# Kernel optimization log

Hardware: AMD Instinct MI355X
Metric: run time of the kernel (lower is better)

## Reference

```python
import jax, jax.numpy as jnp
import numpy as np

EMB_DIM = 256
N_EGO = 8192
N_SIDE = 8192
TOP_K = 16


def setup_inputs() -> dict:
    key = jax.random.key(0)
    ks = jax.random.split(key, 9)
    s = 1.0 / np.sqrt(EMB_DIM)
    return {
        "ego_emb": jax.random.normal(ks[0], (N_EGO, EMB_DIM), jnp.float32),
        "side_emb": jax.random.normal(ks[1], (N_SIDE, EMB_DIM), jnp.float32),
        "rel_emb": jax.random.normal(ks[2], (N_SIDE, EMB_DIM), jnp.float32),
        "Wq": jax.random.uniform(ks[3], (EMB_DIM, EMB_DIM), jnp.float32, -s, s),
        "bq": jax.random.uniform(ks[4], (EMB_DIM,), jnp.float32, -s, s),
        "Wk": jax.random.uniform(ks[5], (EMB_DIM, EMB_DIM), jnp.float32, -s, s),
        "bk": jax.random.uniform(ks[6], (EMB_DIM,), jnp.float32, -s, s),
        "Wv": jax.random.uniform(ks[7], (EMB_DIM, EMB_DIM), jnp.float32, -s, s),
        "bv": jax.random.uniform(ks[8], (EMB_DIM,), jnp.float32, -s, s),
    }


def reference(ego_emb, side_emb, rel_emb, Wq, bq, Wk, bk, Wv, bv):
    # Linear projections (torch nn.Linear: x @ W.T + b)
    q = ego_emb @ Wq.T + bq                      # [N_ego, d]
    k = (side_emb * rel_emb) @ Wk.T + bk         # [N_side, d]
    v = side_emb @ Wv.T + bv                     # [N_side, d]

    scale = jnp.sqrt(jnp.asarray(EMB_DIM, q.dtype))
    attn_scores = (q @ k.T) / scale              # [N_ego, N_side] dense

    k_value = min(TOP_K, attn_scores.shape[-1])
    topk_scores, topk_indices = jax.lax.top_k(attn_scores, k_value)  # [N_ego, K]
    attn_weights = jax.nn.softmax(topk_scores, axis=-1)              # [N_ego, K]

    topk_v = v[topk_indices]                     # gather -> [N_ego, K, d]
    aggregated = jnp.sum(topk_v * attn_weights[..., None], axis=1)   # [N_ego, d]
    return aggregated
```

## Files before the change

kernel.cpp:

```cpp
#include <hip/hip_runtime.h>
#include <hip/hip_bf16.h>


#define EMB 256
#define NEGO 8192
#define NSIDE 8192
#define TOPKK 16
#define NSPLIT 16
#define SPLITLEN (NSIDE / NSPLIT)
#define BM 128
#define BN 32
#define NGRP (SPLITLEN / BN)
#define CAP 8
#define RESCORE 20

typedef _Float16 f16x8 __attribute__((ext_vector_type(8)));
typedef float f32x16 __attribute__((ext_vector_type(16)));

#define NEG_BIG (-3.402823466e38f)

__device__ __forceinline__ void gload_lds16(const _Float16* g, _Float16* l) {
    __builtin_amdgcn_global_load_lds((const __attribute__((address_space(1))) void*)g,
                                     (__attribute__((address_space(3))) void*)l, 16, 0, 0);
}

__device__ __forceinline__ void split8(const float* xv, f16x8& hi, f16x8& lo) {
#pragma unroll
    for (int j = 0; j < 8; ++j) {
        float x = xv[j];
        _Float16 h = (_Float16)x;
        hi[j] = h;
        lo[j] = (_Float16)(x - (float)h);
    }
}

__device__ __forceinline__ unsigned packkey(float s, unsigned gid) {
    unsigned b = __float_as_uint(s);
    b = ((int)b >= 0) ? (b | 0x80000000u) : ~b;
    return (b & 0xFFFFE000u) | (gid ^ 0x1FFFu);
}

__global__ __launch_bounds__(256, 1) void proj_kernel(
    const float* __restrict__ ego, const float* __restrict__ side, const float* __restrict__ rel,
    const float* __restrict__ Wq, const float* __restrict__ bq,
    const float* __restrict__ Wk, const float* __restrict__ bk,
    const float* __restrict__ Wv, const float* __restrict__ bv,
    _Float16* __restrict__ qh, _Float16* __restrict__ ql,
    _Float16* __restrict__ kh, _Float16* __restrict__ kl,
    float* __restrict__ vout)
{
    __shared__ __align__(16) _Float16 Wh[64 * 256];
    __shared__ __align__(16) _Float16 Wl[64 * 256];

    const int z = blockIdx.y;
    const float* X; const float* W; const float* bias;
    if (z == 0)      { X = ego;  W = Wq; bias = bq; }
    else if (z == 1) { X = side; W = Wk; bias = bk; }
    else             { X = side; W = Wv; bias = bv; }

    const int tid = threadIdx.x, lane = tid & 63, wave = tid >> 6;
    const int hk = lane >> 5, r = lane & 31;
    const int arow = blockIdx.x * BM + wave * 32 + r;

    f16x8 ah[16], al[16];
#pragma unroll
    for (int kst = 0; kst < 16; ++kst) {
        float xv[8];
        const float* p = X + arow * EMB + kst * 16 + hk * 8;
        const float4 x0 = *(const float4*)p;
        const float4 x1 = *(const float4*)(p + 4);
        xv[0]=x0.x; xv[1]=x0.y; xv[2]=x0.z; xv[3]=x0.w;
        xv[4]=x1.x; xv[5]=x1.y; xv[6]=x1.z; xv[7]=x1.w;
        if (z == 1) {
            const float* pr = rel + arow * EMB + kst * 16 + hk * 8;
            const float4 r0 = *(const float4*)pr;
            const float4 r1 = *(const float4*)(pr + 4);
            xv[0]*=r0.x; xv[1]*=r0.y; xv[2]*=r0.z; xv[3]*=r0.w;
            xv[4]*=r1.x; xv[5]*=r1.y; xv[6]*=r1.z; xv[7]*=r1.w;
        }
        split8(xv, ah[kst], al[kst]);
    }

    for (int nt = 0; nt < 4; ++nt) {
        __syncthreads();
#pragma unroll
        for (int i = 0; i < 8; ++i) {
            const int rowi = wave * 16 + i * 2 + hk;
            const int c = r;
            const float* wp = W + (nt * 64 + rowi) * EMB + ((c ^ (rowi & 31)) << 3);
            float xv[8];
            const float4 w0 = *(const float4*)wp;
            const float4 w1 = *(const float4*)(wp + 4);
            xv[0]=w0.x; xv[1]=w0.y; xv[2]=w0.z; xv[3]=w0.w;
            xv[4]=w1.x; xv[5]=w1.y; xv[6]=w1.z; xv[7]=w1.w;
            f16x8 h8, l8;
            split8(xv, h8, l8);
            *(f16x8*)&Wh[rowi * 256 + c * 8] = h8;
            *(f16x8*)&Wl[rowi * 256 + c * 8] = l8;
        }
        __syncthreads();

        f32x16 acc0 = {}, acc1 = {};
#pragma unroll
        for (int kst = 0; kst < 16; ++kst) {
            const int cc = kst * 2 + hk;
            const f16x8 bh0 = *(const f16x8*)&Wh[r * 256 + ((cc ^ r) << 3)];
            const f16x8 bl0 = *(const f16x8*)&Wl[r * 256 + ((cc ^ r) << 3)];
            const f16x8 bh1 = *(const f16x8*)&Wh[(32 + r) * 256 + ((cc ^ r) << 3)];
            const f16x8 bl1 = *(const f16x8*)&Wl[(32 + r) * 256 + ((cc ^ r) << 3)];
            acc0 = __builtin_amdgcn_mfma_f32_32x32x16_f16(ah[kst], bh0, acc0, 0, 0, 0);
            acc0 = __builtin_amdgcn_mfma_f32_32x32x16_f16(al[kst], bh0, acc0, 0, 0, 0);
            acc0 = __builtin_amdgcn_mfma_f32_32x32x16_f16(ah[kst], bl0, acc0, 0, 0, 0);
            acc1 = __builtin_amdgcn_mfma_f32_32x32x16_f16(ah[kst], bh1, acc1, 0, 0, 0);
            acc1 = __builtin_amdgcn_mfma_f32_32x32x16_f16(al[kst], bh1, acc1, 0, 0, 0);
            acc1 = __builtin_amdgcn_mfma_f32_32x32x16_f16(ah[kst], bl1, acc1, 0, 0, 0);
        }

#pragma unroll
        for (int reg = 0; reg < 16; ++reg) {
            const int crow = (reg & 3) + 8 * (reg >> 2) + 4 * hk;
            const int grow = blockIdx.x * BM + wave * 32 + crow;
            const int col0 = nt * 64 + r;
            const int col1 = nt * 64 + 32 + r;
            const float v0 = acc0[reg] + bias[col0];
            const float v1 = acc1[reg] + bias[col1];
            if (z < 2) {
                _Float16* oh = (z == 0) ? qh : kh;
                _Float16* ol = (z == 0) ? ql : kl;
                _Float16 h0 = (_Float16)v0;
                oh[grow * EMB + col0] = h0;
                ol[grow * EMB + col0] = (_Float16)(v0 - (float)h0);
                _Float16 h1 = (_Float16)v1;
                oh[grow * EMB + col1] = h1;
                ol[grow * EMB + col1] = (_Float16)(v1 - (float)h1);
            } else {
                vout[grow * EMB + col0] = v0;
                vout[grow * EMB + col1] = v1;
            }
        }
    }
}

__global__ __launch_bounds__(256, 2) void scores_topk_kernel(
    const _Float16* __restrict__ qh,
    const _Float16* __restrict__ kh,
    unsigned* __restrict__ part)
{
    __shared__ __align__(16) _Float16 Bh[BN * 256];
    __shared__ unsigned stk[(CAP + 1) * 256];

    const int tid = threadIdx.x, lane = tid & 63, wave = tid >> 6;
    const int hk = lane >> 5, r = lane & 31;
    const int split = blockIdx.x & 15;
    const int bx = blockIdx.x >> 4;
    const int qbase = bx * BM + wave * 32;
    const int rowoff0 = 4 * hk;
    const int gidbase = split * SPLITLEN;

    unsigned tk[16];
    unsigned curmin = 0u;

    f16x8 ah[16];
#pragma unroll
    for (int kst = 0; kst < 16; ++kst) {
        ah[kst] = *(const f16x8*)(qh + (qbase + r) * EMB + kst * 16 + hk * 8);
    }

    auto minTree = [&]() {
        unsigned m0 = min(tk[0], tk[1]),  m1 = min(tk[2], tk[3]);
        unsigned m2 = min(tk[4], tk[5]),  m3 = min(tk[6], tk[7]);
        unsigned m4 = min(tk[8], tk[9]),  m5 = min(tk[10], tk[11]);
        unsigned m6 = min(tk[12], tk[13]), m7 = min(tk[14], tk[15]);
        m0 = min(m0, m1); m2 = min(m2, m3); m4 = min(m4, m5); m6 = min(m6, m7);
        curmin = min(min(m0, m2), min(m4, m6));
    };

    auto insert = [&](unsigned k) {
        const bool p = k > curmin;
        const unsigned target = p ? curmin : 0xFFFFFFFFu;
#pragma unroll
        for (int j = 0; j < 16; ++j) {
            tk[j] = (tk[j] == target) ? k : tk[j];
        }
        minTree();
    };

    int cnt = 0;
    auto rebuild = [&]() {
        int mc = cnt;
#pragma unroll
        for (int o = 32; o; o >>= 1) { const int t = __shfl_xor(mc, o); mc = t > mc ? t : mc; }
        unsigned v = stk[tid];
        for (int e = 0; e < mc; ++e) {
            const unsigned vn = stk[(e + 1) * 256 + tid];
            insert((e < cnt) ? v : 0u);
            v = vn;
        }
        cnt = 0;
    };

    for (int gi = 0; gi < NGRP; ++gi) {
        const int s0 = gidbase + gi * BN;
#pragma unroll
        for (int i = 0; i < 4; ++i) {
            const int rho0 = wave * 8 + i * 2;
            const int rho = rho0 + hk;
            const int gsrc = (s0 + rho) * EMB + ((r ^ (rho & 31)) << 3);
            gload_lds16(kh + gsrc, &Bh[rho0 * 256]);
        }
        __syncthreads();

        f32x16 acc = {};
#pragma unroll
        for (int kst = 0; kst < 16; ++kst) {
            const int slice = kst * 2 + hk;
            const int addr = r * 256 + ((slice ^ r) << 3);
            const f16x8 k_h = *(const f16x8*)&Bh[addr];
            acc = __builtin_amdgcn_mfma_f32_32x32x16_f16(k_h, ah[kst], acc, 0, 0, 0);
        }

        if (gi == 0) {
#pragma unroll
            for (int j = 0; j < 16; ++j) {
                const unsigned gid = (unsigned)(gidbase + (j & 3) + 8 * (j >> 2) + rowoff0);
                tk[j] = packkey(acc[j], gid);
            }
            minTree();
        } else {
            const int base_col = gidbase + gi * BN + rowoff0;
#pragma unroll
            for (int h = 0; h < 2; ++h) {
#pragma unroll
                for (int jj = 0; jj < 8; ++jj) {
                    const int j = h * 8 + jj;
                    const unsigned gid = (unsigned)(base_col + (j & 3) + 8 * (j >> 2));
                    const unsigned key = packkey(acc[j], gid);
                    const bool p = key > curmin;
                    stk[cnt * 256 + tid] = key;
                    cnt += p ? 1 : 0;
                }
                if (__any(cnt > 0)) rebuild();
            }
        }
        __syncthreads();
    }

    {
        unsigned osv[16];
#pragma unroll
        for (int j = 0; j < 16; ++j) osv[j] = (unsigned)__shfl_xor((int)tk[j], 32);
#pragma unroll
        for (int j = 0; j < 16; ++j) insert(osv[j]);
    }

    if (lane < 32) {
        const int row = qbase + r;
#pragma unroll
        for (int j = 0; j < 16; ++j) {
            part[(row * NSPLIT + split) * TOPKK + j] = tk[j];
        }
    }
}

__global__ __launch_bounds__(256) void merge_kernel(
    const unsigned* __restrict__ part,
    const _Float16* __restrict__ qh, const _Float16* __restrict__ ql,
    const _Float16* __restrict__ kh, const _Float16* __restrict__ kl,
    const float* __restrict__ v, float* __restrict__ out)
{
    __shared__ int   isel[4][RESCORE];
    __shared__ float rsc[4][RESCORE];
    const int tid = threadIdx.x, lane = tid & 63, wave = tid >> 6;
    const int row = blockIdx.x * 4 + wave;

    unsigned c0 = part[row * 256 + lane];
    unsigned c1 = part[row * 256 + 64 + lane];
    unsigned c2 = part[row * 256 + 128 + lane];
    unsigned c3 = part[row * 256 + 192 + lane];

    for (int t = 0; t < RESCORE; ++t) {
        unsigned bs = c0 > c1 ? c0 : c1;
        const unsigned b2 = c2 > c3 ? c2 : c3;
        bs = bs > b2 ? bs : b2;
#pragma unroll
        for (int o = 1; o < 64; o <<= 1) {
            const unsigned os = (unsigned)__shfl_xor((int)bs, o);
            bs = os > bs ? os : bs;
        }
        if (lane == 0) isel[wave][t] = (int)((bs & 0x1FFFu) ^ 0x1FFFu);
        c0 = (c0 == bs) ? 0u : c0;
        c1 = (c1 == bs) ? 0u : c1;
        c2 = (c2 == bs) ? 0u : c2;
        c3 = (c3 == bs) ? 0u : c3;
    }
    __syncthreads();

    const int g = lane >> 4, gl = lane & 15;
    float qr[16];
    {
        const f16x8 qa = *(const f16x8*)(qh + (size_t)row * EMB + gl * 16);
        const f16x8 qb = *(const f16x8*)(qh + (size_t)row * EMB + gl * 16 + 8);
        const f16x8 la = *(const f16x8*)(ql + (size_t)row * EMB + gl * 16);
        const f16x8 lb = *(const f16x8*)(ql + (size_t)row * EMB + gl * 16 + 8);
#pragma unroll
        for (int j = 0; j < 8; ++j) {
            qr[j]     = (float)qa[j] + (float)la[j];
            qr[8 + j] = (float)qb[j] + (float)lb[j];
        }
    }

#pragma unroll
    for (int rd = 0; rd < RESCORE / 4; ++rd) {
        const int cidx = rd * 4 + g;
        const int id = isel[wave][cidx];
        const f16x8 ka = *(const f16x8*)(kh + (size_t)id * EMB + gl * 16);
        const f16x8 kb = *(const f16x8*)(kh + (size_t)id * EMB + gl * 16 + 8);
        const f16x8 ma = *(const f16x8*)(kl + (size_t)id * EMB + gl * 16);
        const f16x8 mb = *(const f16x8*)(kl + (size_t)id * EMB + gl * 16 + 8);
        float p = 0.f;
#pragma unroll
        for (int j = 0; j < 8; ++j) {
            p = fmaf(qr[j],     (float)ka[j] + (float)ma[j], p);
            p = fmaf(qr[8 + j], (float)kb[j] + (float)mb[j], p);
        }
#pragma unroll
        for (int o = 1; o < 16; o <<= 1) p += __shfl_xor(p, o);
        if (gl == 0) rsc[wave][cidx] = p;
    }
    __syncthreads();

    float es = (lane < RESCORE) ? rsc[wave][lane] : NEG_BIG;
    int  eid = (lane < RESCORE) ? isel[wave][lane] : 0x7fffffff;
    float w16[16]; int id16[16];
    float m = 0.f, denom = 0.f;
    for (int t = 0; t < 16; ++t) {
        float bs = es; int bid = eid;
#pragma unroll
        for (int o = 1; o < 64; o <<= 1) {
            const float os = __shfl_xor(bs, o);
            const int oid = __shfl_xor(bid, o);
            if (os > bs || (os == bs && oid < bid)) { bs = os; bid = oid; }
        }
        if (t == 0) m = bs;
        if (eid == bid) { es = NEG_BIG; eid = 0x7fffffff; }
        const float e = expf((bs - m) * 0.0625f);
        w16[t] = e; id16[t] = bid; denom += e;
    }
    const float inv = 1.0f / denom;

    float a0 = 0.f, a1 = 0.f, a2 = 0.f, a3 = 0.f;
#pragma unroll
    for (int t = 0; t < 16; ++t) {
        const float w = w16[t] * inv;
        const float* vp = v + (long)id16[t] * EMB;
        a0 += w * vp[lane];
        a1 += w * vp[lane + 64];
        a2 += w * vp[lane + 128];
        a3 += w * vp[lane + 192];
    }
    out[row * EMB + lane]       = a0;
    out[row * EMB + lane + 64]  = a1;
    out[row * EMB + lane + 128] = a2;
    out[row * EMB + lane + 192] = a3;
}

extern "C" void kernel_launch(void* const* d_in, const int* in_sizes, int n_in,
                              void* d_out, int out_size, void* d_ws, size_t ws_size,
                              hipStream_t stream) {
    (void)in_sizes; (void)n_in; (void)out_size; (void)ws_size;
    const float* ego  = (const float*)d_in[0];
    const float* side = (const float*)d_in[1];
    const float* rel  = (const float*)d_in[2];
    const float* Wq   = (const float*)d_in[3];
    const float* bq   = (const float*)d_in[4];
    const float* Wk   = (const float*)d_in[5];
    const float* bk   = (const float*)d_in[6];
    const float* Wv   = (const float*)d_in[7];
    const float* bv   = (const float*)d_in[8];

    char* ws = (char*)d_ws;
    _Float16* qh = (_Float16*)ws;
    _Float16* ql = qh + (size_t)NEGO * EMB;
    _Float16* kh = ql + (size_t)NEGO * EMB;
    _Float16* kl = kh + (size_t)NSIDE * EMB;
    float*    vbuf = (float*)(ws + 16u * 1024 * 1024);
    unsigned* part = (unsigned*)(ws + 24u * 1024 * 1024);
    float* out = (float*)d_out;

    proj_kernel<<<dim3(NEGO / BM, 3), dim3(256), 0, stream>>>(
        ego, side, rel, Wq, bq, Wk, bk, Wv, bv, qh, ql, kh, kl, vbuf);
    scores_topk_kernel<<<dim3(NEGO / BM * NSPLIT), dim3(256), 0, stream>>>(
        qh, kh, part);
    merge_kernel<<<dim3(NEGO / 4), dim3(256), 0, stream>>>(
        part, qh, ql, kh, kl, vbuf, out);
}
```

Before: 202.5 us.

## Split projection over output column tiles and widen score tile to 64 keys

The projection kernel now launches one block per 64-column output tile via a third grid dimension instead of looping over four tiles inside each block. This gives four times as many blocks to fill the GPU, but each block re-reads and re-splits its input rows. The scores/top-k kernel doubles the key tile width to 64 and computes two MFMA accumulators per group, halving the number of LDS load/sync rounds. It also doubles the candidate stack capacity, which raises LDS use and may lower occupancy.

```diff
diff --git a/kernel.cpp b/kernel.cpp
--- a/kernel.cpp
+++ b/kernel.cpp
@@ -9,9 +9,9 @@
 #define NSPLIT 16
 #define SPLITLEN (NSIDE / NSPLIT)
 #define BM 128
-#define BN 32
+#define BN 64
 #define NGRP (SPLITLEN / BN)
-#define CAP 8
+#define CAP 16
 #define RESCORE 20
 
 typedef _Float16 f16x8 __attribute__((ext_vector_type(8)));
@@ -52,7 +52,8 @@
     __shared__ __align__(16) _Float16 Wh[64 * 256];
     __shared__ __align__(16) _Float16 Wl[64 * 256];
 
-    const int z = blockIdx.y;
+    const int z = blockIdx.z;
+    const int nt = blockIdx.y;
     const float* X; const float* W; const float* bias;
     if (z == 0)      { X = ego;  W = Wq; bias = bq; }
     else if (z == 1) { X = side; W = Wk; bias = bk; }
@@ -81,62 +82,59 @@
         split8(xv, ah[kst], al[kst]);
     }
 
-    for (int nt = 0; nt < 4; ++nt) {
-        __syncthreads();
-#pragma unroll
-        for (int i = 0; i < 8; ++i) {
-            const int rowi = wave * 16 + i * 2 + hk;
-            const int c = r;
-            const float* wp = W + (nt * 64 + rowi) * EMB + ((c ^ (rowi & 31)) << 3);
-            float xv[8];
-            const float4 w0 = *(const float4*)wp;
-            const float4 w1 = *(const float4*)(wp + 4);
-            xv[0]=w0.x; xv[1]=w0.y; xv[2]=w0.z; xv[3]=w0.w;
-            xv[4]=w1.x; xv[5]=w1.y; xv[6]=w1.z; xv[7]=w1.w;
-            f16x8 h8, l8;
-            split8(xv, h8, l8);
-            *(f16x8*)&Wh[rowi * 256 + c * 8] = h8;
-            *(f16x8*)&Wl[rowi * 256 + c * 8] = l8;
-        }
-        __syncthreads();
-
-        f32x16 acc0 = {}, acc1 = {};
-#pragma unroll
-        for (int kst = 0; kst < 16; ++kst) {
-            const int cc = kst * 2 + hk;
-            const f16x8 bh0 = *(const f16x8*)&Wh[r * 256 + ((cc ^ r) << 3)];
-            const f16x8 bl0 = *(const f16x8*)&Wl[r * 256 + ((cc ^ r) << 3)];
-            const f16x8 bh1 = *(const f16x8*)&Wh[(32 + r) * 256 + ((cc ^ r) << 3)];
-            const f16x8 bl1 = *(const f16x8*)&Wl[(32 + r) * 256 + ((cc ^ r) << 3)];
-            acc0 = __builtin_amdgcn_mfma_f32_32x32x16_f16(ah[kst], bh0, acc0, 0, 0, 0);
-            acc0 = __builtin_amdgcn_mfma_f32_32x32x16_f16(al[kst], bh0, acc0, 0, 0, 0);
-            acc0 = __builtin_amdgcn_mfma_f32_32x32x16_f16(ah[kst], bl0, acc0, 0, 0, 0);
-            acc1 = __builtin_amdgcn_mfma_f32_32x32x16_f16(ah[kst], bh1, acc1, 0, 0, 0);
-            acc1 = __builtin_amdgcn_mfma_f32_32x32x16_f16(al[kst], bh1, acc1, 0, 0, 0);
-            acc1 = __builtin_amdgcn_mfma_f32_32x32x16_f16(ah[kst], bl1, acc1, 0, 0, 0);
-        }
-
-#pragma unroll
-        for (int reg = 0; reg < 16; ++reg) {
-            const int crow = (reg & 3) + 8 * (reg >> 2) + 4 * hk;
-            const int grow = blockIdx.x * BM + wave * 32 + crow;
-            const int col0 = nt * 64 + r;
-            const int col1 = nt * 64 + 32 + r;
-            const float v0 = acc0[reg] + bias[col0];
-            const float v1 = acc1[reg] + bias[col1];
-            if (z < 2) {
-                _Float16* oh = (z == 0) ? qh : kh;
-                _Float16* ol = (z == 0) ? ql : kl;
-                _Float16 h0 = (_Float16)v0;
-                oh[grow * EMB + col0] = h0;
-                ol[grow * EMB + col0] = (_Float16)(v0 - (float)h0);
-                _Float16 h1 = (_Float16)v1;
-                oh[grow * EMB + col1] = h1;
-                ol[grow * EMB + col1] = (_Float16)(v1 - (float)h1);
-            } else {
-                vout[grow * EMB + col0] = v0;
-                vout[grow * EMB + col1] = v1;
-            }
+#pragma unroll
+    for (int i = 0; i < 8; ++i) {
+        const int rowi = wave * 16 + i * 2 + hk;
+        const int c = r;
+        const float* wp = W + (nt * 64 + rowi) * EMB + ((c ^ (rowi & 31)) << 3);
+        float xv[8];
+        const float4 w0 = *(const float4*)wp;
+        const float4 w1 = *(const float4*)(wp + 4);
+        xv[0]=w0.x; xv[1]=w0.y; xv[2]=w0.z; xv[3]=w0.w;
+        xv[4]=w1.x; xv[5]=w1.y; xv[6]=w1.z; xv[7]=w1.w;
+        f16x8 h8, l8;
+        split8(xv, h8, l8);
+        *(f16x8*)&Wh[rowi * 256 + c * 8] = h8;
+        *(f16x8*)&Wl[rowi * 256 + c * 8] = l8;
+    }
+    __syncthreads();
+
+    f32x16 acc0 = {}, acc1 = {};
+#pragma unroll
+    for (int kst = 0; kst < 16; ++kst) {
+        const int cc = kst * 2 + hk;
+        const f16x8 bh0 = *(const f16x8*)&Wh[r * 256 + ((cc ^ r) << 3)];
+        const f16x8 bl0 = *(const f16x8*)&Wl[r * 256 + ((cc ^ r) << 3)];
+        const f16x8 bh1 = *(const f16x8*)&Wh[(32 + r) * 256 + ((cc ^ r) << 3)];
+        const f16x8 bl1 = *(const f16x8*)&Wl[(32 + r) * 256 + ((cc ^ r) << 3)];
+        acc0 = __builtin_amdgcn_mfma_f32_32x32x16_f16(ah[kst], bh0, acc0, 0, 0, 0);
+        acc0 = __builtin_amdgcn_mfma_f32_32x32x16_f16(al[kst], bh0, acc0, 0, 0, 0);
+        acc0 = __builtin_amdgcn_mfma_f32_32x32x16_f16(ah[kst], bl0, acc0, 0, 0, 0);
+        acc1 = __builtin_amdgcn_mfma_f32_32x32x16_f16(ah[kst], bh1, acc1, 0, 0, 0);
+        acc1 = __builtin_amdgcn_mfma_f32_32x32x16_f16(al[kst], bh1, acc1, 0, 0, 0);
+        acc1 = __builtin_amdgcn_mfma_f32_32x32x16_f16(ah[kst], bl1, acc1, 0, 0, 0);
+    }
+
+#pragma unroll
+    for (int reg = 0; reg < 16; ++reg) {
+        const int crow = (reg & 3) + 8 * (reg >> 2) + 4 * hk;
+        const int grow = blockIdx.x * BM + wave * 32 + crow;
+        const int col0 = nt * 64 + r;
+        const int col1 = nt * 64 + 32 + r;
+        const float v0 = acc0[reg] + bias[col0];
+        const float v1 = acc1[reg] + bias[col1];
+        if (z < 2) {
+            _Float16* oh = (z == 0) ? qh : kh;
+            _Float16* ol = (z == 0) ? ql : kl;
+            _Float16 h0 = (_Float16)v0;
+            oh[grow * EMB + col0] = h0;
+            ol[grow * EMB + col0] = (_Float16)(v0 - (float)h0);
+            _Float16 h1 = (_Float16)v1;
+            oh[grow * EMB + col1] = h1;
+            ol[grow * EMB + col1] = (_Float16)(v1 - (float)h1);
+        } else {
+            vout[grow * EMB + col0] = v0;
+            vout[grow * EMB + col1] = v1;
         }
     }
 }
@@ -199,48 +197,58 @@
         cnt = 0;
     };
 
+    auto filter8 = [&](const f32x16& acc, int q4, int base_col) {
+#pragma unroll
+        for (int jj = 0; jj < 8; ++jj) {
+            const int j = q4 * 8 + jj;
+            const unsigned gid = (unsigned)(base_col + (j & 3) + 8 * (j >> 2));
+            const unsigned key = packkey(acc[j], gid);
+            const bool p = key > curmin;
+            stk[cnt * 256 + tid] = key;
+            cnt += p ? 1 : 0;
+        }
+    };
+
     for (int gi = 0; gi < NGRP; ++gi) {
         const int s0 = gidbase + gi * BN;
 #pragma unroll
-        for (int i = 0; i < 4; ++i) {
-            const int rho0 = wave * 8 + i * 2;
+        for (int i = 0; i < 8; ++i) {
+            const int rho0 = wave * 16 + i * 2;
             const int rho = rho0 + hk;
             const int gsrc = (s0 + rho) * EMB + ((r ^ (rho & 31)) << 3);
             gload_lds16(kh + gsrc, &Bh[rho0 * 256]);
         }
         __syncthreads();
 
-        f32x16 acc = {};
+        f32x16 acc0 = {}, acc1 = {};
 #pragma unroll
         for (int kst = 0; kst < 16; ++kst) {
             const int slice = kst * 2 + hk;
-            const int addr = r * 256 + ((slice ^ r) << 3);
-            const f16x8 k_h = *(const f16x8*)&Bh[addr];
-            acc = __builtin_amdgcn_mfma_f32_32x32x16_f16(k_h, ah[kst], acc, 0, 0, 0);
-        }
-
+            const f16x8 k0 = *(const f16x8*)&Bh[r * 256 + ((slice ^ r) << 3)];
+            const f16x8 k1 = *(const f16x8*)&Bh[(32 + r) * 256 + ((slice ^ r) << 3)];
+            acc0 = __builtin_amdgcn_mfma_f32_32x32x16_f16(k0, ah[kst], acc0, 0, 0, 0);
+            acc1 = __builtin_amdgcn_mfma_f32_32x32x16_f16(k1, ah[kst], acc1, 0, 0, 0);
+        }
+
+        const int base0 = gidbase + gi * BN + rowoff0;
+        const int base1 = base0 + 32;
         if (gi == 0) {
 #pragma unroll
             for (int j = 0; j < 16; ++j) {
-                const unsigned gid = (unsigned)(gidbase + (j & 3) + 8 * (j >> 2) + rowoff0);
-                tk[j] = packkey(acc[j], gid);
+                const unsigned gid = (unsigned)(base0 + (j & 3) + 8 * (j >> 2));
+                tk[j] = packkey(acc0[j], gid);
             }
             minTree();
+            filter8(acc1, 0, base1);
+            filter8(acc1, 1, base1);
+            if (__any(cnt > 0)) rebuild();
         } else {
-            const int base_col = gidbase + gi * BN + rowoff0;
-#pragma unroll
-            for (int h = 0; h < 2; ++h) {
-#pragma unroll
-                for (int jj = 0; jj < 8; ++jj) {
-                    const int j = h * 8 + jj;
-                    const unsigned gid = (unsigned)(base_col + (j & 3) + 8 * (j >> 2));
-                    const unsigned key = packkey(acc[j], gid);
-                    const bool p = key > curmin;
-                    stk[cnt * 256 + tid] = key;
-                    cnt += p ? 1 : 0;
-                }
-                if (__any(cnt > 0)) rebuild();
-            }
+            filter8(acc0, 0, base0);
+            filter8(acc0, 1, base0);
+            if (__any(cnt > 0)) rebuild();
+            filter8(acc1, 0, base1);
+            filter8(acc1, 1, base1);
+            if (__any(cnt > 0)) rebuild();
         }
         __syncthreads();
     }
@@ -387,7 +395,7 @@
     unsigned* part = (unsigned*)(ws + 24u * 1024 * 1024);
     float* out = (float*)d_out;
 
-    proj_kernel<<<dim3(NEGO / BM, 3), dim3(256), 0, stream>>>(
+    proj_kernel<<<dim3(NEGO / BM, 4, 3), dim3(256), 0, stream>>>(
         ego, side, rel, Wq, bq, Wk, bk, Wv, bv, qh, ql, kh, kl, vbuf);
     scores_topk_kernel<<<dim3(NEGO / BM * NSPLIT), dim3(256), 0, stream>>>(
         qh, kh, part);
```

Measured after the change: 182.0 us. -10.1%, faster.
